# Optimization experiments

Hardware: AMD Instinct MI355X
Metric: run time of the kernel (lower is better)

The kernel has to match this reference:

```python
import jax, jax.numpy as jnp
import numpy as np

N_NODES = 100000
N_EDGES = 3200000
N_FEAT = 128
N_GRAPHS = 256
N_CLASSES = 10


def setup_inputs() -> dict:
    key = jax.random.key(0)
    ks = jax.random.split(key, 10)
    x = jax.random.normal(ks[0], (N_NODES, N_FEAT), dtype=jnp.float32)
    edge_index = jax.random.randint(ks[1], (2, N_EDGES), 0, N_NODES, dtype=jnp.int64)
    batch = jnp.sort(jax.random.randint(ks[2], (N_NODES,), 0, N_GRAPHS, dtype=jnp.int64))
    # GCNConv weights (glorot-ish scaling) and biases
    W1 = jax.random.normal(ks[3], (N_FEAT, 16), dtype=jnp.float32) / np.sqrt(N_FEAT)
    b1 = jnp.zeros((16,), dtype=jnp.float32)
    W2 = jax.random.normal(ks[4], (16, 32), dtype=jnp.float32) / np.sqrt(16.0)
    b2 = jnp.zeros((32,), dtype=jnp.float32)
    Wfc = jax.random.normal(ks[5], (32, N_CLASSES), dtype=jnp.float32) / np.sqrt(32.0)
    bfc = jnp.zeros((N_CLASSES,), dtype=jnp.float32)
    return {"x": x, "edge_index": edge_index, "batch": batch,
            "W1": W1, "b1": b1, "W2": W2, "b2": b2, "Wfc": Wfc, "bfc": bfc}


def reference(x, edge_index, batch, W1, b1, W2, b2, Wfc, bfc):
    N = x.shape[0]
    # --- GCN normalization with self-loops (PyG GCNConv default) ---
    loop = jnp.arange(N, dtype=edge_index.dtype)
    src = jnp.concatenate([edge_index[0], loop])  # [E+N]
    dst = jnp.concatenate([edge_index[1], loop])  # [E+N]
    ones = jnp.ones_like(src, dtype=x.dtype)
    deg = jax.ops.segment_sum(ones, dst, num_segments=N)  # in-degree incl self-loop
    dinv = jax.lax.rsqrt(deg)  # deg >= 1 thanks to self-loops
    norm = dinv[src] * dinv[dst]  # [E+N]

    def gcn_conv(h, W, b):
        h = h @ W                               # [N, out] linear first (small out dim)
        msg = h[src] * norm[:, None]            # gather + edge-wise scale
        agg = jax.ops.segment_sum(msg, dst, num_segments=N)  # scatter-add
        return agg + b

    h = jax.nn.relu(gcn_conv(x, W1, b1))
    h = jax.nn.relu(gcn_conv(h, W2, b2))

    # --- global mean pool over graphs ---
    g_sum = jax.ops.segment_sum(h, batch, num_segments=N_GRAPHS)  # [G, 32]
    g_cnt = jax.ops.segment_sum(jnp.ones((N,), dtype=h.dtype), batch, num_segments=N_GRAPHS)
    pooled = g_sum / jnp.maximum(g_cnt, 1.0)[:, None]

    return pooled @ Wfc + bfc  # [G, num_classes]
```

## Files before the change

### kernel.cpp

```cpp
#include <hip/hip_runtime.h>
#include <hip/hip_fp16.h>

#define NF   128
#define C1   16
#define C2   32
#define NCLS 10
#define BSH  8
#define BN   256
#define MAXB 512
#define S    9216
#define TILE 4096
#define EPT  (TILE/256)
#define CAP  12288


struct BinSh { int hist[MAXB]; int off0[MAXB]; int cur[MAXB]; };
struct LinSh { float ws[NF * C1]; float xs[16 * 132]; };
union FatSh { BinSh b; LinSh l; };

__global__ __launch_bounds__(256) void k_fat(const int* __restrict__ ei,
                                             int* __restrict__ packed,
                                             int* __restrict__ offmat,
                                             const float* __restrict__ x,
                                             const float* __restrict__ W1,
                                             __half* __restrict__ y1h,
                                             int E, int nbuck, int nblkA, int N) {
    __shared__ FatSh sm;
    int tid = threadIdx.x;

    if (blockIdx.x < nblkA) {
        long long t0 = (long long)blockIdx.x * TILE;
        for (int i = tid; i < MAXB; i += 256) sm.b.hist[i] = 0;
        __syncthreads();

        int dstv[EPT], srcv[EPT];
#pragma unroll
        for (int u = 0; u < EPT; ++u) {
            long long e = t0 + tid + u * 256;
            int d = -1, s = 0;
            if (e < E) { d = ei[E + e]; s = ei[e]; }
            dstv[u] = d; srcv[u] = s;
            if (d >= 0) atomicAdd(&sm.b.hist[d >> BSH], 1);
        }
        __syncthreads();
        if (tid < 64) {
            int carry = 0;
            for (int c = 0; c < MAXB / 64; ++c) {
                int idx = c * 64 + tid;
                int v = sm.b.hist[idx];
                int orig = v;
                for (int off = 1; off < 64; off <<= 1) {
                    int t = __shfl_up(v, off);
                    if (tid >= off) v += t;
                }
                int ex = v - orig + carry;
                sm.b.off0[idx] = ex;
                sm.b.cur[idx] = ex;
                carry += __shfl(v, 63);
            }
        }
        __syncthreads();
        int* orow = offmat + (size_t)blockIdx.x * (nbuck + 1);
        for (int b = tid; b <= nbuck; b += 256) orow[b] = sm.b.off0[b];
#pragma unroll
        for (int u = 0; u < EPT; ++u) {
            int d = dstv[u];
            if (d >= 0) {
                int b = d >> BSH;
                int slot = atomicAdd(&sm.b.cur[b], 1);
                packed[t0 + slot] = srcv[u] | ((d & (BN - 1)) << 17);
            }
        }
    } else {
        int bid = blockIdx.x - nblkA;
        for (int t = tid; t < NF * C1; t += 256) sm.l.ws[t] = W1[t];
        int n0 = bid * 16;
        const float4* x4 = (const float4*)x;
        for (int t = tid; t < 16 * 32; t += 256) {
            int r = t >> 5, c = t & 31;
            int n = n0 + r;
            float4 v = (n < N) ? x4[(size_t)n * 32 + c] : make_float4(0.f, 0.f, 0.f, 0.f);
            float* d = &sm.l.xs[r * 132 + c * 4];
            d[0] = v.x; d[1] = v.y; d[2] = v.z; d[3] = v.w;
        }
        __syncthreads();
        int r = tid >> 4, j = tid & 15;
        float acc = 0.0f;
#pragma unroll 4
        for (int k = 0; k < NF; ++k) acc += sm.l.xs[r * 132 + k] * sm.l.ws[k * C1 + j];
        int n = n0 + r;
        if (n < N) y1h[(size_t)n * C1 + j] = __float2half_rn(acc);
    }
}


__global__ __launch_bounds__(1024) void k_csr(const int* __restrict__ packed,
                                              const int* __restrict__ offmat,
                                              int* __restrict__ csr,
                                              int* __restrict__ rowptr,
                                              int* __restrict__ deg,
                                              float* __restrict__ dinv,
                                              __half* __restrict__ y1h,
                                              int N, int nbuck, int nblkA) {
    __shared__ int stage[CAP];
    __shared__ int startA[1024];
    __shared__ int spsA[1024];
    __shared__ int o1A[1024];
    __shared__ int hcnt[BN];
    __shared__ int sh[BN];
    __shared__ int cur[BN];
    __shared__ float fdinv[BN];
    int tid = threadIdx.x;
    int b = blockIdx.x;
    size_t base = (size_t)b * S;

    int len = 0, o1 = 0;
    if (tid < nblkA) {
        const int* orow = offmat + (size_t)tid * (nbuck + 1) + b;
        o1 = orow[0];
        len = orow[1] - o1;
    }
    o1A[tid] = o1;
    spsA[tid] = len;
    if (tid < BN) hcnt[tid] = 0;
    __syncthreads();
    for (int off = 1; off < 1024; off <<= 1) {
        int t = (tid >= off) ? spsA[tid - off] : 0;
        __syncthreads();
        spsA[tid] += t;
        __syncthreads();
    }
    int m = spsA[1023];
    startA[tid] = spsA[tid] - len;
    __syncthreads();
    if (m > CAP) m = CAP;

    for (int i = tid; i < m; i += 1024) {
        int lo = 0, hi = 1023;
        while (lo < hi) {
            int mid = (lo + hi + 1) >> 1;
            if (startA[mid] <= i) lo = mid; else hi = mid - 1;
        }
        int p = packed[(size_t)lo * TILE + o1A[lo] + (i - startA[lo])];
        stage[i] = p;
        atomicAdd(&hcnt[p >> 17], 1);
    }
    __syncthreads();
    int v = 0;
    if (tid < BN) { v = hcnt[tid]; sh[tid] = v; }
    __syncthreads();
    for (int off = 1; off < BN; off <<= 1) {
        int t = (tid < BN && tid >= off) ? sh[tid - off] : 0;
        __syncthreads();
        if (tid < BN) sh[tid] += t;
        __syncthreads();
    }
    if (tid < BN) {
        int ex = sh[tid] - v;
        cur[tid] = ex;
        float dv = rsqrtf((float)v + 1.0f);
        fdinv[tid] = dv;
        int n = (b << BSH) + tid;
        if (n < N) {
            rowptr[n] = (int)base + ex;
            deg[n] = v;
            dinv[n] = dv;
        }
    }
    __syncthreads();
    for (int i = tid; i < m; i += 1024) {
        int p = stage[i];
        int slot = atomicAdd(&cur[p >> 17], 1);
        csr[base + slot] = p & 0x1FFFF;
    }
    int n0 = b << BSH;
    int lim = min(BN, N - n0);
    if (lim > 0) {
        __half2* yrow = (__half2*)y1h + (size_t)n0 * 8;
        int tot = lim * 8;
        for (int i = tid; i < tot; i += 1024) {
            float dv = fdinv[i >> 3];
            float2 f = __half22float2(yrow[i]);
            yrow[i] = __floats2half2_rn(f.x * dv, f.y * dv);
        }
    }
}


template <int MODE>
__global__ __launch_bounds__(256) void k_gather_h(const int* __restrict__ rowptr,
                                                  const int* __restrict__ deg,
                                                  const int* __restrict__ csr,
                                                  const float* __restrict__ dinv,
                                                  const float* __restrict__ bias,
                                                  const uint2* __restrict__ yh,
                                                  void* __restrict__ outp, int N) {
    int tid = threadIdx.x;
    int j = tid & 3;
    int n = blockIdx.x * 64 + (tid >> 2);
    if (n >= N) return;
    int k0 = rowptr[n];
    int k1 = k0 + deg[n];
    union U { uint2 u; __half2 h[2]; };
    U su; su.u = yh[(size_t)n * 4 + j];
    float2 sl = __half22float2(su.h[0]), shh = __half22float2(su.h[1]);
    float a0 = sl.x, a1 = sl.y, a2 = shh.x, a3 = shh.y;
    float b0 = 0.f, b1v = 0.f, b2 = 0.f, b3 = 0.f;
    int k = k0;
    for (; k + 3 < k1; k += 4) {
        int s0 = csr[k], s1 = csr[k + 1], s2 = csr[k + 2], s3 = csr[k + 3];
        U v0, v1, v2, v3;
        v0.u = yh[(size_t)s0 * 4 + j];
        v1.u = yh[(size_t)s1 * 4 + j];
        v2.u = yh[(size_t)s2 * 4 + j];
        v3.u = yh[(size_t)s3 * 4 + j];
        float2 l0 = __half22float2(v0.h[0]), h0 = __half22float2(v0.h[1]);
        float2 l1 = __half22float2(v1.h[0]), h1 = __half22float2(v1.h[1]);
        float2 l2 = __half22float2(v2.h[0]), h2 = __half22float2(v2.h[1]);
        float2 l3 = __half22float2(v3.h[0]), h3 = __half22float2(v3.h[1]);
        a0 += l0.x; a1 += l0.y; a2 += h0.x; a3 += h0.y;
        b0 += l1.x; b1v += l1.y; b2 += h1.x; b3 += h1.y;
        a0 += l2.x; a1 += l2.y; a2 += h2.x; a3 += h2.y;
        b0 += l3.x; b1v += l3.y; b2 += h3.x; b3 += h3.y;
    }
    for (; k < k1; ++k) {
        U v; v.u = yh[(size_t)csr[k] * 4 + j];
        float2 l = __half22float2(v.h[0]), h = __half22float2(v.h[1]);
        a0 += l.x; a1 += l.y; a2 += h.x; a3 += h.y;
    }
    float dn = dinv[n];
    float r0 = dn * (a0 + b0), r1 = dn * (a1 + b1v);
    float r2 = dn * (a2 + b2), r3 = dn * (a3 + b3);
    if (MODE == 0) {
        ((float4*)outp)[(size_t)n * 4 + j] = make_float4(r0, r1, r2, r3);
    } else {
        float4 bb = ((const float4*)bias)[j];
        U o;
        o.h[0] = __floats2half2_rn(fmaxf(r0 + bb.x, 0.0f) * dn, fmaxf(r1 + bb.y, 0.0f) * dn);
        o.h[1] = __floats2half2_rn(fmaxf(r2 + bb.z, 0.0f) * dn, fmaxf(r3 + bb.w, 0.0f) * dn);
        ((uint2*)outp)[(size_t)n * 4 + j] = o.u;
    }
}


__global__ __launch_bounds__(256) void k_pool_fc(const float* __restrict__ z,
                                                 const float* __restrict__ W2,
                                                 const float* __restrict__ b2,
                                                 const int* __restrict__ batch,
                                                 const float* __restrict__ Wfc,
                                                 const float* __restrict__ bfc,
                                                 float* __restrict__ out, int N, int G) {
    __shared__ float W2s[C1 * C2];
    int tid = threadIdx.x;
    for (int t = tid; t < C1 * C2; t += 256) W2s[t] = W2[t];

    int g = blockIdx.x;
    int lo = 0, hi = N;
    while (lo < hi) { int m = (lo + hi) >> 1; if (batch[m] < g) lo = m + 1; else hi = m; }
    int start = lo;
    lo = start; hi = N;
    while (lo < hi) { int m = (lo + hi) >> 1; if (batch[m] < g + 1) lo = m + 1; else hi = m; }
    int end = lo;
    __syncthreads();

    int i = tid & 31, r = tid >> 5;
    float bi = b2[i];
    float acc = 0.0f;
    for (int n = start + r; n < end; n += 8) {
        const float* zr = &z[(size_t)n * C1];
        float h = bi;
#pragma unroll
        for (int j = 0; j < C1; ++j) h += zr[j] * W2s[j * C2 + i];
        acc += fmaxf(h, 0.0f);
    }

    __shared__ float red[256];
    red[tid] = acc;
    __syncthreads();
    for (int s = 4; s >= 1; s >>= 1) {
        if (r < s) red[tid] += red[tid + s * 32];
        __syncthreads();
    }
    __shared__ float pooled[C2];
    if (tid < C2) {
        float cnt = (float)(end - start);
        pooled[tid] = red[tid] / fmaxf(cnt, 1.0f);
    }
    __syncthreads();
    if (tid < NCLS) {
        float a = bfc[tid];
#pragma unroll
        for (int j = 0; j < C2; ++j) a += pooled[j] * Wfc[j * NCLS + tid];
        out[g * NCLS + tid] = a;
    }
}

extern "C" void kernel_launch(void* const* d_in, const int* in_sizes, int n_in,
                              void* d_out, int out_size, void* d_ws, size_t ws_size,
                              hipStream_t stream) {
    const float* x    = (const float*)d_in[0];
    const int*   ei   = (const int*)d_in[1];
    const int*   batch= (const int*)d_in[2];
    const float* W1   = (const float*)d_in[3];
    const float* b1   = (const float*)d_in[4];
    const float* W2   = (const float*)d_in[5];
    const float* b2   = (const float*)d_in[6];
    const float* Wfc  = (const float*)d_in[7];
    const float* bfc  = (const float*)d_in[8];
    float* out = (float*)d_out;

    const int N = in_sizes[0] / NF;
    const int E = in_sizes[1] / 2;
    const int G = out_size / NCLS;
    const int nbuck = (N + BN - 1) >> BSH;
    const int nblkA = (E + TILE - 1) / TILE;
    const int nblkL = (N + 15) / 16;

    char* p = (char*)d_ws;
    auto alloc = [&](size_t bytes) { char* q = p; p += (bytes + 63) & ~(size_t)63; return q; };
    int*     rowptr  = (int*)    alloc((size_t)N * 4);
    int*     deg     = (int*)    alloc((size_t)N * 4);
    float*   dinv    = (float*)  alloc((size_t)N * 4);
    int*     packed  = (int*)    alloc((size_t)nblkA * TILE * 4);
    int*     offmat  = (int*)    alloc((size_t)nblkA * (nbuck + 1) * 4);
    int*     csr     = (int*)    alloc((size_t)nbuck * S * 4);
    __half*  y1h     = (__half*) alloc((size_t)N * C1 * 2);
    __half*  uh      = (__half*) alloc((size_t)N * C1 * 2);
    float*   z       = (float*)  alloc((size_t)N * C1 * 4);

    const int B = 256;

    k_fat<<<nblkA + nblkL, B, 0, stream>>>(ei, packed, offmat, x, W1, y1h,
                                           E, nbuck, nblkA, N);
    k_csr<<<nbuck, 1024, 0, stream>>>(packed, offmat, csr, rowptr, deg, dinv, y1h,
                                      N, nbuck, nblkA);

    k_gather_h<1><<<(N + 63) / 64, B, 0, stream>>>(rowptr, deg, csr, dinv, b1,
                                                   (const uint2*)y1h, uh, N);
    k_gather_h<0><<<(N + 63) / 64, B, 0, stream>>>(rowptr, deg, csr, dinv, b1,
                                                   (const uint2*)uh, z, N);

    k_pool_fc<<<G, B, 0, stream>>>(z, W2, b2, batch, Wfc, bfc, out, N, G);
}
```

Baseline: 173.2 us.

## Split fused bin/linear kernel, halve bin tile, re-read packed edges in CSR

Splits the fused binning+first-linear kernel into two separate launches (k_bin and k_lin1). It halves the edge tile so there are twice as many binning blocks, and extends the CSR kernel's per-bucket run scan to 2048 runs. The CSR build no longer stages each bucket's edges in a 48KB shared buffer. It re-reads them from global memory in a second pass, with a second binary search per element. This lowers shared-memory use and removes the CAP truncation, at the cost of an extra kernel launch and more global reads and searches.

```diff
diff --git a/kernel.cpp b/kernel.cpp
--- a/kernel.cpp
+++ b/kernel.cpp
@@ -9,87 +9,61 @@
 #define BN   256
 #define MAXB 512
 #define S    9216
-#define TILE 4096
+#define TILE 2048
 #define EPT  (TILE/256)
-#define CAP  12288
-
-
-struct BinSh { int hist[MAXB]; int off0[MAXB]; int cur[MAXB]; };
-struct LinSh { float ws[NF * C1]; float xs[16 * 132]; };
-union FatSh { BinSh b; LinSh l; };
-
-__global__ __launch_bounds__(256) void k_fat(const int* __restrict__ ei,
+#define NRUN 2048
+
+
+__global__ __launch_bounds__(256) void k_bin(const int* __restrict__ ei,
                                              int* __restrict__ packed,
                                              int* __restrict__ offmat,
-                                             const float* __restrict__ x,
-                                             const float* __restrict__ W1,
-                                             __half* __restrict__ y1h,
-                                             int E, int nbuck, int nblkA, int N) {
-    __shared__ FatSh sm;
-    int tid = threadIdx.x;
-
-    if (blockIdx.x < nblkA) {
-        long long t0 = (long long)blockIdx.x * TILE;
-        for (int i = tid; i < MAXB; i += 256) sm.b.hist[i] = 0;
-        __syncthreads();
-
-        int dstv[EPT], srcv[EPT];
+                                             int E, int nbuck) {
+    __shared__ int hist[MAXB];
+    __shared__ int off0[MAXB];
+    __shared__ int cur[MAXB];
+    int tid = threadIdx.x;
+    long long t0 = (long long)blockIdx.x * TILE;
+
+    for (int i = tid; i < MAXB; i += 256) hist[i] = 0;
+    __syncthreads();
+
+    int dstv[EPT], srcv[EPT];
 #pragma unroll
-        for (int u = 0; u < EPT; ++u) {
-            long long e = t0 + tid + u * 256;
-            int d = -1, s = 0;
-            if (e < E) { d = ei[E + e]; s = ei[e]; }
-            dstv[u] = d; srcv[u] = s;
-            if (d >= 0) atomicAdd(&sm.b.hist[d >> BSH], 1);
-        }
-        __syncthreads();
-        if (tid < 64) {
-            int carry = 0;
-            for (int c = 0; c < MAXB / 64; ++c) {
-                int idx = c * 64 + tid;
-                int v = sm.b.hist[idx];
-                int orig = v;
-                for (int off = 1; off < 64; off <<= 1) {
-                    int t = __shfl_up(v, off);
-                    if (tid >= off) v += t;
-                }
-                int ex = v - orig + carry;
-                sm.b.off0[idx] = ex;
-                sm.b.cur[idx] = ex;
-                carry += __shfl(v, 63);
+    for (int u = 0; u < EPT; ++u) {
+        long long e = t0 + tid + u * 256;
+        int d = -1, s = 0;
+        if (e < E) { d = ei[E + e]; s = ei[e]; }
+        dstv[u] = d; srcv[u] = s;
+        if (d >= 0) atomicAdd(&hist[d >> BSH], 1);
+    }
+    __syncthreads();
+    if (tid < 64) {
+        int carry = 0;
+        for (int c = 0; c < MAXB / 64; ++c) {
+            int idx = c * 64 + tid;
+            int v = hist[idx];
+            int orig = v;
+            for (int off = 1; off < 64; off <<= 1) {
+                int t = __shfl_up(v, off);
+                if (tid >= off) v += t;
             }
-        }
-        __syncthreads();
-        int* orow = offmat + (size_t)blockIdx.x * (nbuck + 1);
-        for (int b = tid; b <= nbuck; b += 256) orow[b] = sm.b.off0[b];
+            int ex = v - orig + carry;
+            off0[idx] = ex;
+            cur[idx] = ex;
+            carry += __shfl(v, 63);
+        }
+    }
+    __syncthreads();
+    int* orow = offmat + (size_t)blockIdx.x * (nbuck + 1);
+    for (int b = tid; b <= nbuck; b += 256) orow[b] = off0[b];
 #pragma unroll
-        for (int u = 0; u < EPT; ++u) {
-            int d = dstv[u];
-            if (d >= 0) {
-                int b = d >> BSH;
-                int slot = atomicAdd(&sm.b.cur[b], 1);
-                packed[t0 + slot] = srcv[u] | ((d & (BN - 1)) << 17);
-            }
-        }
-    } else {
-        int bid = blockIdx.x - nblkA;
-        for (int t = tid; t < NF * C1; t += 256) sm.l.ws[t] = W1[t];
-        int n0 = bid * 16;
-        const float4* x4 = (const float4*)x;
-        for (int t = tid; t < 16 * 32; t += 256) {
-            int r = t >> 5, c = t & 31;
-            int n = n0 + r;
-            float4 v = (n < N) ? x4[(size_t)n * 32 + c] : make_float4(0.f, 0.f, 0.f, 0.f);
-            float* d = &sm.l.xs[r * 132 + c * 4];
-            d[0] = v.x; d[1] = v.y; d[2] = v.z; d[3] = v.w;
-        }
-        __syncthreads();
-        int r = tid >> 4, j = tid & 15;
-        float acc = 0.0f;
-#pragma unroll 4
-        for (int k = 0; k < NF; ++k) acc += sm.l.xs[r * 132 + k] * sm.l.ws[k * C1 + j];
-        int n = n0 + r;
-        if (n < N) y1h[(size_t)n * C1 + j] = __float2half_rn(acc);
+    for (int u = 0; u < EPT; ++u) {
+        int d = dstv[u];
+        if (d >= 0) {
+            int b = d >> BSH;
+            int slot = atomicAdd(&cur[b], 1);
+            packed[t0 + slot] = srcv[u] | ((d & (BN - 1)) << 17);
+        }
     }
 }
 
@@ -102,61 +76,74 @@
                                               float* __restrict__ dinv,
                                               __half* __restrict__ y1h,
                                               int N, int nbuck, int nblkA) {
-    __shared__ int stage[CAP];
-    __shared__ int startA[1024];
-    __shared__ int spsA[1024];
-    __shared__ int o1A[1024];
+    __shared__ int startA[NRUN];
+    __shared__ int o1A[NRUN];
     __shared__ int hcnt[BN];
-    __shared__ int sh[BN];
+    __shared__ int sh2[BN];
     __shared__ int cur[BN];
     __shared__ float fdinv[BN];
     int tid = threadIdx.x;
     int b = blockIdx.x;
     size_t base = (size_t)b * S;
 
-    int len = 0, o1 = 0;
-    if (tid < nblkA) {
-        const int* orow = offmat + (size_t)tid * (nbuck + 1) + b;
-        o1 = orow[0];
-        len = orow[1] - o1;
-    }
-    o1A[tid] = o1;
-    spsA[tid] = len;
+    int len0 = 0, len1 = 0;
+    {
+        int o = 0, L = 0;
+        if (tid < nblkA) {
+            const int* orow = offmat + (size_t)tid * (nbuck + 1) + b;
+            o = orow[0]; L = orow[1] - o;
+        }
+        o1A[tid] = o; startA[tid] = L; len0 = L;
+    }
+    {
+        int idx = 1024 + tid, o = 0, L = 0;
+        if (idx < nblkA) {
+            const int* orow = offmat + (size_t)idx * (nbuck + 1) + b;
+            o = orow[0]; L = orow[1] - o;
+        }
+        o1A[idx] = o; startA[idx] = L; len1 = L;
+    }
     if (tid < BN) hcnt[tid] = 0;
     __syncthreads();
     for (int off = 1; off < 1024; off <<= 1) {
-        int t = (tid >= off) ? spsA[tid - off] : 0;
-        __syncthreads();
-        spsA[tid] += t;
-        __syncthreads();
-    }
-    int m = spsA[1023];
-    startA[tid] = spsA[tid] - len;
-    __syncthreads();
-    if (m > CAP) m = CAP;
+        int a0 = (tid >= off) ? startA[tid - off] : 0;
+        int a1 = (tid >= off) ? startA[1024 + tid - off] : 0;
+        __syncthreads();
+        if (tid >= off) { startA[tid] += a0; startA[1024 + tid] += a1; }
+        __syncthreads();
+    }
+    int c0 = startA[1023];
+    startA[1024 + tid] += c0;
+    __syncthreads();
+    int m = startA[NRUN - 1];
+    int e0 = startA[tid] - len0;
+    int e1 = startA[1024 + tid] - len1;
+    __syncthreads();
+    startA[tid] = e0;
+    startA[1024 + tid] = e1;
+    __syncthreads();
 
     for (int i = tid; i < m; i += 1024) {
-        int lo = 0, hi = 1023;
+        int lo = 0, hi = NRUN - 1;
         while (lo < hi) {
             int mid = (lo + hi + 1) >> 1;
             if (startA[mid] <= i) lo = mid; else hi = mid - 1;
         }
         int p = packed[(size_t)lo * TILE + o1A[lo] + (i - startA[lo])];
-        stage[i] = p;
         atomicAdd(&hcnt[p >> 17], 1);
     }
     __syncthreads();
     int v = 0;
-    if (tid < BN) { v = hcnt[tid]; sh[tid] = v; }
+    if (tid < BN) { v = hcnt[tid]; sh2[tid] = v; }
     __syncthreads();
     for (int off = 1; off < BN; off <<= 1) {
-        int t = (tid < BN && tid >= off) ? sh[tid - off] : 0;
-        __syncthreads();
-        if (tid < BN) sh[tid] += t;
+        int t = (tid < BN && tid >= off) ? sh2[tid - off] : 0;
+        __syncthreads();
+        if (tid < BN) sh2[tid] += t;
         __syncthreads();
     }
     if (tid < BN) {
-        int ex = sh[tid] - v;
+        int ex = sh2[tid] - v;
         cur[tid] = ex;
         float dv = rsqrtf((float)v + 1.0f);
         fdinv[tid] = dv;
@@ -169,7 +156,12 @@
     }
     __syncthreads();
     for (int i = tid; i < m; i += 1024) {
-        int p = stage[i];
+        int lo = 0, hi = NRUN - 1;
+        while (lo < hi) {
+            int mid = (lo + hi + 1) >> 1;
+            if (startA[mid] <= i) lo = mid; else hi = mid - 1;
+        }
+        int p = packed[(size_t)lo * TILE + o1A[lo] + (i - startA[lo])];
         int slot = atomicAdd(&cur[p >> 17], 1);
         csr[base + slot] = p & 0x1FFFF;
     }
@@ -184,6 +176,32 @@
             yrow[i] = __floats2half2_rn(f.x * dv, f.y * dv);
         }
     }
+}
+
+
+__global__ __launch_bounds__(256) void k_lin1(const float* __restrict__ x,
+                                              const float* __restrict__ W1,
+                                              __half* __restrict__ y1h, int N) {
+    __shared__ float ws[NF * C1];
+    __shared__ float xs[16 * 132];
+    int tid = threadIdx.x;
+    for (int t = tid; t < NF * C1; t += 256) ws[t] = W1[t];
+    int n0 = blockIdx.x * 16;
+    const float4* x4 = (const float4*)x;
+    for (int t = tid; t < 16 * 32; t += 256) {
+        int r = t >> 5, c = t & 31;
+        int n = n0 + r;
+        float4 v = (n < N) ? x4[(size_t)n * 32 + c] : make_float4(0.f, 0.f, 0.f, 0.f);
+        float* d = &xs[r * 132 + c * 4];
+        d[0] = v.x; d[1] = v.y; d[2] = v.z; d[3] = v.w;
+    }
+    __syncthreads();
+    int r = tid >> 4, j = tid & 15;
+    float acc = 0.0f;
+#pragma unroll 4
+    for (int k = 0; k < NF; ++k) acc += xs[r * 132 + k] * ws[k * C1 + j];
+    int n = n0 + r;
+    if (n < N) y1h[(size_t)n * C1 + j] = __float2half_rn(acc);
 }
 
 
@@ -314,7 +332,6 @@
     const int G = out_size / NCLS;
     const int nbuck = (N + BN - 1) >> BSH;
     const int nblkA = (E + TILE - 1) / TILE;
-    const int nblkL = (N + 15) / 16;
 
     char* p = (char*)d_ws;
     auto alloc = [&](size_t bytes) { char* q = p; p += (bytes + 63) & ~(size_t)63; return q; };
@@ -330,8 +347,8 @@
 
     const int B = 256;
 
-    k_fat<<<nblkA + nblkL, B, 0, stream>>>(ei, packed, offmat, x, W1, y1h,
-                                           E, nbuck, nblkA, N);
+    k_bin<<<nblkA, B, 0, stream>>>(ei, packed, offmat, E, nbuck);
+    k_lin1<<<(N + 15) / 16, B, 0, stream>>>(x, W1, y1h, N);
     k_csr<<<nbuck, 1024, 0, stream>>>(packed, offmat, csr, rowptr, deg, dinv, y1h,
                                       N, nbuck, nblkA);
 
```

Result: slower. 183.3 us (+5.8%).
